# Performance work log

Hardware: AMD Instinct MI355X
Metric: run time of the kernel (lower is better)

Reference implementation:

```python
import jax, jax.numpy as jnp
import numpy as np

N_NODES = 8192
EMBED = 64
N_NEURONS = [512, 256, 128]
ACTION_SIZE = 8
BATCH = 4096


def setup_inputs() -> dict:
    key = jax.random.key(0)
    ks = jax.random.split(key, 16)
    in_size = 2 * N_NODES + 2 * EMBED

    def u(k, shape, bound):
        return jax.random.uniform(k, shape, jnp.float32, -bound, bound)

    stdv1 = 1.0 / np.sqrt(N_NEURONS[0])
    stdv2 = 1.0 / np.sqrt(EMBED)
    return {
        "state": jax.random.uniform(ks[0], (N_NODES, N_NODES), jnp.float32),
        "start": jax.random.randint(ks[1], (BATCH,), 0, N_NODES),
        "end": jax.random.randint(ks[2], (BATCH,), 0, N_NODES),
        # GCN layer params
        "gw1": u(ks[3], (1, N_NEURONS[0]), stdv1),
        "gb1": u(ks[4], (N_NEURONS[0],), stdv1),
        "gw2": u(ks[5], (N_NEURONS[0], EMBED), stdv2),
        "gb2": u(ks[6], (EMBED,), stdv2),
        # dense head params (xavier-ish)
        "fw1": u(ks[7], (in_size, N_NEURONS[0]), np.sqrt(6.0 / (in_size + N_NEURONS[0]))),
        "fb1": jnp.zeros((N_NEURONS[0],), jnp.float32),
        "fw2": u(ks[8], (N_NEURONS[0], N_NEURONS[1]), np.sqrt(6.0 / (N_NEURONS[0] + N_NEURONS[1]))),
        "fb2": jnp.zeros((N_NEURONS[1],), jnp.float32),
        "fw3": u(ks[9], (N_NEURONS[1], N_NEURONS[2]), np.sqrt(6.0 / (N_NEURONS[1] + N_NEURONS[2]))),
        "fb3": jnp.zeros((N_NEURONS[2],), jnp.float32),
        "fw4": u(ks[10], (N_NEURONS[2], ACTION_SIZE), np.sqrt(6.0 / (N_NEURONS[2] + ACTION_SIZE))),
        "fb4": jnp.zeros((ACTION_SIZE,), jnp.float32),
    }


def reference(state, start, end, gw1, gb1, gw2, gb2,
              fw1, fb1, fw2, fb2, fw3, fb3, fw4, fb4):
    # x = diag(state) as [N, 1] node features
    x = jnp.diagonal(state)[:, None]
    # adj = state with zeroed diagonal, detached (no grad through adj)
    adj = jax.lax.stop_gradient(jnp.fill_diagonal(state, 0.0, inplace=False))
    # GCN layer 1: relu(adj @ (x @ W) + b); dropout is identity in eval mode
    h = jax.nn.relu(adj @ (x @ gw1) + gb1)              # [N, 512]
    # GCN layer 2
    h = jax.nn.relu(adj @ (h @ gw2) + gb2)              # [N, 64]
    h = jax.nn.log_softmax(h, axis=1)                   # [N, 64]
    # gather node features and embeddings for each (start, end) edge
    edge_features = jnp.concatenate(
        [state[start], state[end], h[start], h[end]], axis=1)  # [B, 2N+2E]
    y = jax.nn.relu(edge_features @ fw1 + fb1)
    y = jax.nn.relu(y @ fw2 + fb2)                      # d1 dropout: identity (eval)
    y = jax.nn.relu(y @ fw3 + fb3)
    action_q = jax.nn.relu(y @ fw4 + fb4)               # [B, action_size]
    return action_q
```

## Files before the change

kernel.cpp:

```cpp
#include <hip/hip_runtime.h>
#include <hip/hip_bf16.h>
#include <math.h>

#define NN 8192
#define EMB 64
#define H1D 512
#define NB 4096

typedef __bf16 bf16x8 __attribute__((ext_vector_type(8)));
typedef float f32x4 __attribute__((ext_vector_type(4)));
typedef unsigned short u16x8 __attribute__((ext_vector_type(8)));
typedef unsigned short u16x4 __attribute__((ext_vector_type(4)));

__device__ __forceinline__ unsigned short f2bf(float f) {
    return __bfloat16_as_ushort(__float2bfloat16(f));
}

__device__ __forceinline__ void gload16(const void* g, void* l) {
    __builtin_amdgcn_global_load_lds(
        (const __attribute__((address_space(1))) void*)g,
        (__attribute__((address_space(3))) void*)l, 16, 0, 0);
}

__global__ void k_diag(const float* __restrict__ state, float* __restrict__ diag) {
    int i = blockIdx.x * blockDim.x + threadIdx.x;
    if (i < NN) diag[i] = state[(size_t)i * NN + i];
}

__global__ __launch_bounds__(256) void k_convert(const float* __restrict__ state,
                                                 const float* __restrict__ diag,
                                                 unsigned short* __restrict__ stateb,
                                                 float* __restrict__ s) {
    int row = blockIdx.x;
    int tid = threadIdx.x;
    const float4* st4 = (const float4*)(state + (size_t)row * NN);
    const float4* dg4 = (const float4*)diag;
    unsigned short* drow = stateb + (size_t)row * NN;
    float acc = 0.f;
#pragma unroll
    for (int t = 0; t < 8; ++t) {
        int f = t * 256 + tid;
        float4 a = st4[f], d = dg4[f];
        acc += a.x * d.x + a.y * d.y + a.z * d.z + a.w * d.w;
        u16x4 o;
        o[0] = f2bf(a.x); o[1] = f2bf(a.y); o[2] = f2bf(a.z); o[3] = f2bf(a.w);
        *(u16x4*)&drow[f * 4] = o;
    }
#pragma unroll
    for (int m = 32; m >= 1; m >>= 1) acc += __shfl_xor(acc, m);
    __shared__ float red[4];
    if ((tid & 63) == 0) red[tid >> 6] = acc;
    __syncthreads();
    if (tid == 0) {
        float tot = red[0] + red[1] + red[2] + red[3];
        float d = diag[row];
        s[row] = tot - d * d;
    }
}

__global__ __launch_bounds__(256) void k_tr_fw1(const float* __restrict__ fw1,
                                                unsigned short* __restrict__ fw1t) {
    __shared__ float t[64][65];
    int kb = blockIdx.x * 64, nb = blockIdx.y * 64;
    int tid = threadIdx.x;
#pragma unroll
    for (int i = 0; i < 4; ++i) {
        int lin = i * 256 + tid;
        int r = lin >> 4, c4 = (lin & 15) << 2;
        float4 v = *(const float4*)&fw1[(size_t)(kb + r) * 512 + nb + c4];
        t[r][c4] = v.x; t[r][c4 + 1] = v.y; t[r][c4 + 2] = v.z; t[r][c4 + 3] = v.w;
    }
    __syncthreads();
#pragma unroll
    for (int i = 0; i < 4; ++i) {
        int lin = i * 256 + tid;
        int n = lin >> 4, k4 = (lin & 15) << 2;
        u16x4 o;
        o[0] = f2bf(t[k4 + 0][n]); o[1] = f2bf(t[k4 + 1][n]);
        o[2] = f2bf(t[k4 + 2][n]); o[3] = f2bf(t[k4 + 3][n]);
        *(u16x4*)&fw1t[(size_t)(nb + n) * 16512 + kb + k4] = o;
    }
}

__global__ __launch_bounds__(256) void k_tr_q(const float* __restrict__ q,
                                              unsigned short* __restrict__ qbT) {
    __shared__ float t[64][65];
    int kb = blockIdx.x * 64;
    int tid = threadIdx.x;
#pragma unroll
    for (int i = 0; i < 4; ++i) {
        int lin = i * 256 + tid;
        int r = lin >> 4, c4 = (lin & 15) << 2;
        float4 v = *(const float4*)&q[(size_t)(kb + r) * 64 + c4];
        t[r][c4] = v.x; t[r][c4 + 1] = v.y; t[r][c4 + 2] = v.z; t[r][c4 + 3] = v.w;
    }
    __syncthreads();
#pragma unroll
    for (int i = 0; i < 4; ++i) {
        int lin = i * 256 + tid;
        int c = lin >> 4, k4 = (lin & 15) << 2;
        u16x4 o;
        o[0] = f2bf(t[k4 + 0][c]); o[1] = f2bf(t[k4 + 1][c]);
        o[2] = f2bf(t[k4 + 2][c]); o[3] = f2bf(t[k4 + 3][c]);
        *(u16x4*)&qbT[(size_t)c * 8192 + kb + k4] = o;
    }
}

__global__ __launch_bounds__(256) void k_rowdot(const float* __restrict__ state,
                                                const float* __restrict__ diag,
                                                float* __restrict__ s) {
    int row = blockIdx.x;
    int tid = threadIdx.x;
    const float4* st4 = (const float4*)(state + (size_t)row * NN);
    const float4* dg4 = (const float4*)diag;
    float acc = 0.f;
#pragma unroll
    for (int t = 0; t < 8; ++t) {
        int f = t * 256 + tid;
        float4 a = st4[f], d = dg4[f];
        acc += a.x * d.x + a.y * d.y + a.z * d.z + a.w * d.w;
    }
#pragma unroll
    for (int m = 32; m >= 1; m >>= 1) acc += __shfl_xor(acc, m);
    __shared__ float red[4];
    if ((tid & 63) == 0) red[tid >> 6] = acc;
    __syncthreads();
    if (tid == 0) {
        float tot = red[0] + red[1] + red[2] + red[3];
        float d = diag[row];
        s[row] = tot - d * d;
    }
}

__global__ __launch_bounds__(256) void k_q(const float* __restrict__ s,
                                           const float* __restrict__ gw1,
                                           const float* __restrict__ gb1,
                                           const float* __restrict__ gw2,
                                           float* __restrict__ q) {
    int tid = threadIdx.x;
    int c = tid & 63;
    int row = blockIdx.x * 4 + (tid >> 6);
    float sv = s[row];
    float a0 = 0.f, a1 = 0.f, a2 = 0.f, a3 = 0.f;
    for (int j = 0; j < H1D; j += 4) {
        float h0 = fmaxf(fmaf(sv, gw1[j + 0], gb1[j + 0]), 0.f);
        float h1 = fmaxf(fmaf(sv, gw1[j + 1], gb1[j + 1]), 0.f);
        float h2 = fmaxf(fmaf(sv, gw1[j + 2], gb1[j + 2]), 0.f);
        float h3 = fmaxf(fmaf(sv, gw1[j + 3], gb1[j + 3]), 0.f);
        a0 = fmaf(h0, gw2[(j + 0) * EMB + c], a0);
        a1 = fmaf(h1, gw2[(j + 1) * EMB + c], a1);
        a2 = fmaf(h2, gw2[(j + 2) * EMB + c], a2);
        a3 = fmaf(h3, gw2[(j + 3) * EMB + c], a3);
    }
    q[row * EMB + c] = (a0 + a1) + (a2 + a3);
}


__global__ __launch_bounds__(256) void k_gcn2_mfma_b(const unsigned short* __restrict__ stateb,
                                                     const unsigned short* __restrict__ qbT,
                                                     float* __restrict__ partg) {
    __shared__ __align__(16) unsigned short Asm[2][64 * 64];
    __shared__ __align__(16) unsigned short Bsm[2][64 * 64];
    const int tid = threadIdx.x;
    const int l = tid & 63, wv = tid >> 6;
    const int rbase = blockIdx.x * 64;
    const int kbase0 = blockIdx.y * 1024;

    const unsigned short* aP[2]; const unsigned short* bP[2]; int lb[2];
#pragma unroll
    for (int i = 0; i < 2; ++i) {
        int slot = i * 256 + tid;
        int r = slot >> 3, cg = slot & 7;
        aP[i] = stateb + (size_t)(rbase + r) * NN + kbase0 + ((cg ^ (r & 7)) << 3);
        bP[i] = qbT + (size_t)r * 8192 + kbase0 + ((cg ^ (r & 7)) << 3);
        lb[i] = (i * 256 + wv * 64) * 8;
    }

    f32x4 acc[4] = {};
    const int fr = l & 15, fq = l >> 4;

#pragma unroll
    for (int i = 0; i < 2; ++i) {
        gload16(aP[i], &Asm[0][lb[i]]);
        gload16(bP[i], &Bsm[0][lb[i]]);
    }
    __syncthreads();

    int buf = 0;
    for (int kt = 0; kt < 16; ++kt) {
        if (kt < 15) {
#pragma unroll
            for (int i = 0; i < 2; ++i) {
                gload16(aP[i] + (kt + 1) * 64, &Asm[buf ^ 1][lb[i]]);
                gload16(bP[i] + (kt + 1) * 64, &Bsm[buf ^ 1][lb[i]]);
            }
        }
#pragma unroll
        for (int kh = 0; kh < 2; ++kh) {
            int ch = kh * 4 + fq;
            int row = wv * 16 + fr;
            bf16x8 aF = *(const bf16x8*)&Asm[buf][row * 64 + ((ch ^ (row & 7)) << 3)];
            bf16x8 bF[4];
#pragma unroll
            for (int n = 0; n < 4; ++n) {
                int col = n * 16 + fr;
                bF[n] = *(const bf16x8*)&Bsm[buf][col * 64 + ((ch ^ (col & 7)) << 3)];
            }
#pragma unroll
            for (int n = 0; n < 4; ++n)
                acc[n] = __builtin_amdgcn_mfma_f32_16x16x32_bf16(aF, bF[n], acc[n], 0, 0, 0);
        }
        __syncthreads();
        buf ^= 1;
    }

    float* dst = partg + (size_t)blockIdx.y * (NN * EMB);
#pragma unroll
    for (int n = 0; n < 4; ++n) {
        int row0 = rbase + wv * 16 + fq * 4;
        int col = n * 16 + fr;
#pragma unroll
        for (int j = 0; j < 4; ++j)
            dst[(size_t)(row0 + j) * EMB + col] = acc[n][j];
    }
}

__global__ __launch_bounds__(256) void k_gcn2_combine_b(const float* __restrict__ partg,
                                                        const float* __restrict__ diag,
                                                        const float* __restrict__ q,
                                                        const float* __restrict__ gb2,
                                                        unsigned short* __restrict__ hb) {
    int tid = threadIdx.x;
    int c = tid & 63;
    int row = blockIdx.x * 4 + (tid >> 6);
    int idx = row * EMB + c;
    float v = gb2[c] - diag[row] * q[idx];
#pragma unroll
    for (int p = 0; p < 8; ++p) v += partg[(size_t)p * NN * EMB + idx];
    v = fmaxf(v, 0.f);
    float mx = v;
#pragma unroll
    for (int m = 32; m >= 1; m >>= 1) mx = fmaxf(mx, __shfl_xor(mx, m));
    float e = expf(v - mx);
    float sum = e;
#pragma unroll
    for (int m = 32; m >= 1; m >>= 1) sum += __shfl_xor(sum, m);
    hb[idx] = f2bf(v - mx - logf(sum));
}

__global__ __launch_bounds__(256) void k_head1_mfma_b(
    const unsigned short* __restrict__ stateb, const unsigned short* __restrict__ hb,
    const int* __restrict__ start, const int* __restrict__ end,
    const unsigned short* __restrict__ fw1t, float* __restrict__ parth) {
    __shared__ __align__(16) unsigned short Asm[128 * 64];
    __shared__ __align__(16) unsigned short Bsm[128 * 64];
    __shared__ int ridx[128];
    const int tid = threadIdx.x;
    const int l = tid & 63, wv = tid >> 6;
    const int rbase = blockIdx.x * 128, cbase = blockIdx.y * 128;
    const int ks = blockIdx.z, side = ks >> 1, half = ks & 1;
    if (tid < 128) ridx[tid] = (side ? end : start)[rbase + tid];
    __syncthreads();

    const unsigned short* aS[4]; const unsigned short* aH[4];
    const unsigned short* bP[4];
    unsigned short* aL[4]; unsigned short* bL[4];
#pragma unroll
    for (int i = 0; i < 4; ++i) {
        int slot = i * 256 + tid;
        int r = slot >> 3, cg = slot & 7;
        int swz = (cg ^ (r & 7)) << 3;
        int gi = ridx[r];
        aS[i] = stateb + (size_t)gi * NN + half * 4096 + swz;
        aH[i] = hb + gi * EMB + swz;
        bP[i] = fw1t + (size_t)(cbase + r) * 16512 + swz;
        aL[i] = &Asm[slot * 8];
        bL[i] = &Bsm[slot * 8];
    }
    const int kB0 = side * 8192 + half * 4096;
    const int kBtail = 16384 + side * 64;
    const int nsteps = 64 + half;

    f32x4 acc[4][4] = {};
    const int wm = wv >> 1, wn = wv & 1;
    const int fr = l & 15, fq = l >> 4;

    for (int kt = 0; kt < nsteps; ++kt) {
        if (kt < 64) {
#pragma unroll
            for (int i = 0; i < 4; ++i) {
                gload16(aS[i] + kt * 64, aL[i]);
                gload16(bP[i] + kB0 + kt * 64, bL[i]);
            }
        } else {
#pragma unroll
            for (int i = 0; i < 4; ++i) {
                gload16(aH[i], aL[i]);
                gload16(bP[i] + kBtail, bL[i]);
            }
        }
        __syncthreads();
#pragma unroll
        for (int kh = 0; kh < 2; ++kh) {
            int ch = kh * 4 + fq;
            bf16x8 aF[4], bF[4];
#pragma unroll
            for (int m = 0; m < 4; ++m) {
                int row = wm * 64 + m * 16 + fr;
                aF[m] = *(const bf16x8*)&Asm[row * 64 + ((ch ^ (row & 7)) << 3)];
            }
#pragma unroll
            for (int n = 0; n < 4; ++n) {
                int nl = wn * 64 + n * 16 + fr;
                bF[n] = *(const bf16x8*)&Bsm[nl * 64 + ((ch ^ (nl & 7)) << 3)];
            }
#pragma unroll
            for (int m = 0; m < 4; ++m)
#pragma unroll
                for (int n = 0; n < 4; ++n)
                    acc[m][n] = __builtin_amdgcn_mfma_f32_16x16x32_bf16(
                        aF[m], bF[n], acc[m][n], 0, 0, 0);
        }
        __syncthreads();
    }

    float* dst = parth + (size_t)ks * (NB * H1D);
#pragma unroll
    for (int m = 0; m < 4; ++m) {
        int row0 = rbase + wm * 64 + m * 16 + fq * 4;
#pragma unroll
        for (int n = 0; n < 4; ++n) {
            int col = cbase + wn * 64 + n * 16 + fr;
#pragma unroll
            for (int j = 0; j < 4; ++j)
                dst[(size_t)(row0 + j) * H1D + col] = acc[m][n][j];
        }
    }
}

__global__ void k_head1_fin4(const float* __restrict__ parth, const float* __restrict__ fb1,
                             float* __restrict__ y1) {
    int i = blockIdx.x * blockDim.x + threadIdx.x;
    const size_t S = (size_t)NB * H1D;
    float4 a = *(const float4*)&parth[(size_t)i * 4];
    float4 b = *(const float4*)&parth[S + (size_t)i * 4];
    float4 c = *(const float4*)&parth[2 * S + (size_t)i * 4];
    float4 d = *(const float4*)&parth[3 * S + (size_t)i * 4];
    float4 bias = *(const float4*)&fb1[(i * 4) & 511];
    float4 o;
    o.x = fmaxf(a.x + b.x + c.x + d.x + bias.x, 0.f);
    o.y = fmaxf(a.y + b.y + c.y + d.y + bias.y, 0.f);
    o.z = fmaxf(a.z + b.z + c.z + d.z + bias.z, 0.f);
    o.w = fmaxf(a.w + b.w + c.w + d.w + bias.w, 0.f);
    *(float4*)&y1[(size_t)i * 4] = o;
}


__global__ __launch_bounds__(256) void k_gcn2_mfma(const float* __restrict__ state,
                                                   const unsigned short* __restrict__ qbT,
                                                   float* __restrict__ partg) {
    __shared__ __align__(16) unsigned short Asm[2][64 * 64];
    __shared__ __align__(16) unsigned short Bsm[2][64 * 64];
    const int tid = threadIdx.x;
    const int l = tid & 63, wv = tid >> 6;
    const int rbase = blockIdx.x * 64;
    const int kbase0 = blockIdx.y * 1024;

    const float* aptr[2]; int awr[2];
#pragma unroll
    for (int i = 0; i < 2; ++i) {
        int slot = i * 256 + tid;
        int r = slot >> 3, cg = slot & 7;
        aptr[i] = state + (size_t)(rbase + r) * NN + kbase0 + cg * 8;
        awr[i] = r * 64 + ((cg ^ (r & 7)) << 3);
    }
    const unsigned short* bptr[2]; int bbase[2];
#pragma unroll
    for (int i = 0; i < 2; ++i) {
        int c = i * 32 + wv * 8 + (l >> 3);
        int cg = l & 7;
        bptr[i] = qbT + (size_t)c * 8192 + kbase0 + ((cg ^ (c & 7)) << 3);
        bbase[i] = i * 2048 + wv * 512;
    }

    f32x4 acc[4] = {};
    const int fr = l & 15, fq = l >> 4;
    float4 va[2][2];

#pragma unroll
    for (int i = 0; i < 2; ++i) {
        va[i][0] = *(const float4*)aptr[i];
        va[i][1] = *(const float4*)(aptr[i] + 4);
    }
#pragma unroll
    for (int i = 0; i < 2; ++i) {
        u16x8 o;
        o[0] = f2bf(va[i][0].x); o[1] = f2bf(va[i][0].y); o[2] = f2bf(va[i][0].z); o[3] = f2bf(va[i][0].w);
        o[4] = f2bf(va[i][1].x); o[5] = f2bf(va[i][1].y); o[6] = f2bf(va[i][1].z); o[7] = f2bf(va[i][1].w);
        *(u16x8*)&Asm[0][awr[i]] = o;
        gload16(bptr[i], &Bsm[0][bbase[i]]);
    }
    __syncthreads();

    int buf = 0;
    for (int kt = 0; kt < 16; ++kt) {
        if (kt < 15) {
#pragma unroll
            for (int i = 0; i < 2; ++i) {
                gload16(bptr[i] + (kt + 1) * 64, &Bsm[buf ^ 1][bbase[i]]);
                va[i][0] = *(const float4*)(aptr[i] + (kt + 1) * 64);
                va[i][1] = *(const float4*)(aptr[i] + (kt + 1) * 64 + 4);
            }
        }
#pragma unroll
        for (int kh = 0; kh < 2; ++kh) {
            int ch = kh * 4 + fq;
            int row = wv * 16 + fr;
            bf16x8 aF = *(const bf16x8*)&Asm[buf][row * 64 + ((ch ^ (row & 7)) << 3)];
            bf16x8 bF[4];
#pragma unroll
            for (int n = 0; n < 4; ++n) {
                int col = n * 16 + fr;
                bF[n] = *(const bf16x8*)&Bsm[buf][col * 64 + ((ch ^ (col & 7)) << 3)];
            }
#pragma unroll
            for (int n = 0; n < 4; ++n)
                acc[n] = __builtin_amdgcn_mfma_f32_16x16x32_bf16(aF, bF[n], acc[n], 0, 0, 0);
        }
        if (kt < 15) {
#pragma unroll
            for (int i = 0; i < 2; ++i) {
                u16x8 o;
                o[0] = f2bf(va[i][0].x); o[1] = f2bf(va[i][0].y); o[2] = f2bf(va[i][0].z); o[3] = f2bf(va[i][0].w);
                o[4] = f2bf(va[i][1].x); o[5] = f2bf(va[i][1].y); o[6] = f2bf(va[i][1].z); o[7] = f2bf(va[i][1].w);
                *(u16x8*)&Asm[buf ^ 1][awr[i]] = o;
            }
        }
        __syncthreads();
        buf ^= 1;
    }

    float* dst = partg + (size_t)blockIdx.y * (NN * EMB);
#pragma unroll
    for (int n = 0; n < 4; ++n) {
        int row0 = rbase + wv * 16 + fq * 4;
        int col = n * 16 + fr;
#pragma unroll
        for (int j = 0; j < 4; ++j)
            dst[(size_t)(row0 + j) * EMB + col] = acc[n][j];
    }
}

__global__ __launch_bounds__(256) void k_gcn2_combine(const float* __restrict__ partg,
                                                      const float* __restrict__ diag,
                                                      const float* __restrict__ q,
                                                      const float* __restrict__ gb2,
                                                      float* __restrict__ h) {
    int tid = threadIdx.x;
    int c = tid & 63;
    int row = blockIdx.x * 4 + (tid >> 6);
    int idx = row * EMB + c;
    float v = gb2[c] - diag[row] * q[idx];
#pragma unroll
    for (int p = 0; p < 8; ++p) v += partg[(size_t)p * NN * EMB + idx];
    v = fmaxf(v, 0.f);
    float mx = v;
#pragma unroll
    for (int m = 32; m >= 1; m >>= 1) mx = fmaxf(mx, __shfl_xor(mx, m));
    float e = expf(v - mx);
    float sum = e;
#pragma unroll
    for (int m = 32; m >= 1; m >>= 1) sum += __shfl_xor(sum, m);
    h[idx] = v - mx - logf(sum);
}

__global__ __launch_bounds__(256) void k_head1_mfma(
    const float* __restrict__ state, const float* __restrict__ h,
    const int* __restrict__ start, const int* __restrict__ end,
    const unsigned short* __restrict__ fw1t, float* __restrict__ part) {
    __shared__ __align__(16) unsigned short Asm[2][64 * 64];
    __shared__ __align__(16) unsigned short Bsm[2][128 * 64];
    __shared__ int ridx[64];
    const int tid = threadIdx.x;
    const int l = tid & 63, wv = tid >> 6;
    const int rbase = blockIdx.x * 64, cbase = blockIdx.y * 128;
    const int ks = blockIdx.z;
    if (tid < 64) ridx[tid] = (ks ? end : start)[rbase + tid];
    __syncthreads();

    const float* aptr[2]; const float* hptr[2]; int awr[2];
#pragma unroll
    for (int i = 0; i < 2; ++i) {
        int slot = i * 256 + tid;
        int r = slot >> 3, cg = slot & 7;
        int gi = ridx[r];
        aptr[i] = state + (size_t)gi * NN + cg * 8;
        hptr[i] = h + gi * EMB + cg * 8;
        awr[i] = r * 64 + ((cg ^ (r & 7)) << 3);
    }
    const unsigned short* bptr[4]; int bbase[4];
#pragma unroll
    for (int i = 0; i < 4; ++i) {
        int n = i * 32 + wv * 8 + (l >> 3);
        int cg = l & 7;
        bptr[i] = fw1t + (size_t)(cbase + n) * 16512 + ((cg ^ (n & 7)) << 3);
        bbase[i] = i * 2048 + wv * 512;
    }

    f32x4 acc[2][4] = {};
    const int wm = wv >> 1, wn = wv & 1;
    const int fr = l & 15, fq = l >> 4;
    float4 va[2][2];

#pragma unroll
    for (int i = 0; i < 2; ++i) {
        va[i][0] = *(const float4*)aptr[i];
        va[i][1] = *(const float4*)(aptr[i] + 4);
    }
#pragma unroll
    for (int i = 0; i < 2; ++i) {
        u16x8 o;
        o[0] = f2bf(va[i][0].x); o[1] = f2bf(va[i][0].y); o[2] = f2bf(va[i][0].z); o[3] = f2bf(va[i][0].w);
        o[4] = f2bf(va[i][1].x); o[5] = f2bf(va[i][1].y); o[6] = f2bf(va[i][1].z); o[7] = f2bf(va[i][1].w);
        *(u16x8*)&Asm[0][awr[i]] = o;
    }
#pragma unroll
    for (int i = 0; i < 4; ++i) gload16(bptr[i] + ks * 8192, &Bsm[0][bbase[i]]);
    __syncthreads();

    int buf = 0;
    for (int kt = 0; kt < 129; ++kt) {
        if (kt < 128) {
            int nxt = kt + 1;
            int kB = (nxt < 128) ? (ks * 8192 + nxt * 64) : (16384 + ks * 64);
#pragma unroll
            for (int i = 0; i < 4; ++i) gload16(bptr[i] + kB, &Bsm[buf ^ 1][bbase[i]]);
#pragma unroll
            for (int i = 0; i < 2; ++i) {
                const float* src = (nxt < 128) ? (aptr[i] + nxt * 64) : hptr[i];
                va[i][0] = *(const float4*)src;
                va[i][1] = *(const float4*)(src + 4);
            }
        }
#pragma unroll
        for (int kh = 0; kh < 2; ++kh) {
            int ch = kh * 4 + fq;
            bf16x8 aF[2], bF[4];
#pragma unroll
            for (int m = 0; m < 2; ++m) {
                int row = wm * 32 + m * 16 + fr;
                aF[m] = *(const bf16x8*)&Asm[buf][row * 64 + ((ch ^ (row & 7)) << 3)];
            }
#pragma unroll
            for (int n = 0; n < 4; ++n) {
                int nl = wn * 64 + n * 16 + fr;
                bF[n] = *(const bf16x8*)&Bsm[buf][nl * 64 + ((ch ^ (nl & 7)) << 3)];
            }
#pragma unroll
            for (int m = 0; m < 2; ++m)
#pragma unroll
                for (int n = 0; n < 4; ++n)
                    acc[m][n] = __builtin_amdgcn_mfma_f32_16x16x32_bf16(
                        aF[m], bF[n], acc[m][n], 0, 0, 0);
        }
        if (kt < 128) {
#pragma unroll
            for (int i = 0; i < 2; ++i) {
                u16x8 o;
                o[0] = f2bf(va[i][0].x); o[1] = f2bf(va[i][0].y); o[2] = f2bf(va[i][0].z); o[3] = f2bf(va[i][0].w);
                o[4] = f2bf(va[i][1].x); o[5] = f2bf(va[i][1].y); o[6] = f2bf(va[i][1].z); o[7] = f2bf(va[i][1].w);
                *(u16x8*)&Asm[buf ^ 1][awr[i]] = o;
            }
        }
        __syncthreads();
        buf ^= 1;
    }

    float* dst = part + (size_t)ks * (NB * H1D);
#pragma unroll
    for (int m = 0; m < 2; ++m) {
        int row0 = rbase + wm * 32 + m * 16 + fq * 4;
#pragma unroll
        for (int n = 0; n < 4; ++n) {
            int col = cbase + wn * 64 + n * 16 + fr;
#pragma unroll
            for (int j = 0; j < 4; ++j)
                dst[(size_t)(row0 + j) * H1D + col] = acc[m][n][j];
        }
    }
}

__global__ void k_head1_fin(const float* __restrict__ part, const float* __restrict__ fb1,
                            float* __restrict__ y1) {
    int i = blockIdx.x * blockDim.x + threadIdx.x;
    float4 a = *(const float4*)&part[(size_t)i * 4];
    float4 b = *(const float4*)&part[(size_t)NB * H1D + (size_t)i * 4];
    float4 bias = *(const float4*)&fb1[(i * 4) & 511];
    float4 o;
    o.x = fmaxf(a.x + b.x + bias.x, 0.f);
    o.y = fmaxf(a.y + b.y + bias.y, 0.f);
    o.z = fmaxf(a.z + b.z + bias.z, 0.f);
    o.w = fmaxf(a.w + b.w + bias.w, 0.f);
    *(float4*)&y1[(size_t)i * 4] = o;
}

#define GEMM_INNER(AsM, BsM)                                          \
    _Pragma("unroll")                                                 \
    for (int k4 = 0; k4 < 64; k4 += 4) {                              \
        float av[4][4], bv[4][4];                                     \
        _Pragma("unroll")                                             \
        for (int i = 0; i < 4; ++i)                                   \
            *(float4*)av[i] = *(const float4*)&AsM[4 * row_t + i][k4];\
        _Pragma("unroll")                                             \
        for (int t = 0; t < 4; ++t)                                   \
            *(float4*)bv[t] = *(const float4*)&BsM[k4 + t][4 * col_t];\
        _Pragma("unroll")                                             \
        for (int i = 0; i < 4; ++i) {                                 \
            _Pragma("unroll")                                         \
            for (int t = 0; t < 4; ++t) {                             \
                _Pragma("unroll")                                     \
                for (int j = 0; j < 4; ++j)                           \
                    acc[i][j] = fmaf(av[i][t], bv[t][j], acc[i][j]);  \
            }                                                         \
        }                                                             \
    }

__global__ __launch_bounds__(256) void k_gemm_relu(const float* __restrict__ A,
                                                   const float* __restrict__ W,
                                                   const float* __restrict__ bias,
                                                   float* __restrict__ C,
                                                   int M, int N, int K) {
    __shared__ __align__(16) float As[64][68];
    __shared__ __align__(16) float Bs[64][68];
    int tid = threadIdx.x;
    int rbase = blockIdx.x * 64;
    int cbase = blockIdx.y * 64;
    int row_t = tid >> 4, col_t = tid & 15;
    float acc[4][4] = {};
    for (int kt = 0; kt < K / 64; ++kt) {
        int kbase = kt * 64;
#pragma unroll
        for (int l = 0; l < 4; ++l) {
            int lin = l * 256 + tid;
            int r = lin >> 4, k4 = (lin & 15) << 2;
            float4 v = *(const float4*)&A[(size_t)(rbase + r) * K + kbase + k4];
            As[r][k4 + 0] = v.x; As[r][k4 + 1] = v.y; As[r][k4 + 2] = v.z; As[r][k4 + 3] = v.w;
            float4 w = *(const float4*)&W[(size_t)(kbase + r) * N + cbase + k4];
            Bs[r][k4 + 0] = w.x; Bs[r][k4 + 1] = w.y; Bs[r][k4 + 2] = w.z; Bs[r][k4 + 3] = w.w;
        }
        __syncthreads();
        GEMM_INNER(As, Bs)
        __syncthreads();
    }
#pragma unroll
    for (int i = 0; i < 4; ++i) {
        int row = rbase + 4 * row_t + i;
        int col = cbase + 4 * col_t;
        float4 v;
        v.x = fmaxf(acc[i][0] + bias[col + 0], 0.f);
        v.y = fmaxf(acc[i][1] + bias[col + 1], 0.f);
        v.z = fmaxf(acc[i][2] + bias[col + 2], 0.f);
        v.w = fmaxf(acc[i][3] + bias[col + 3], 0.f);
        *(float4*)&C[(size_t)row * N + col] = v;
    }
}

__global__ void k_head4(const float* __restrict__ y3, const float* __restrict__ fw4,
                        const float* __restrict__ fb4, float* __restrict__ out) {
    int tid = blockIdx.x * blockDim.x + threadIdx.x;
    int b = tid >> 3, j = tid & 7;
    float acc = fb4[j];
    for (int k = 0; k < 128; ++k)
        acc = fmaf(y3[b * 128 + k], fw4[k * 8 + j], acc);
    out[tid] = fmaxf(acc, 0.f);
}

extern "C" void kernel_launch(void* const* d_in, const int* in_sizes, int n_in,
                              void* d_out, int out_size, void* d_ws, size_t ws_size,
                              hipStream_t stream) {
    const float* state = (const float*)d_in[0];
    const int* start   = (const int*)d_in[1];
    const int* end     = (const int*)d_in[2];
    const float* gw1   = (const float*)d_in[3];
    const float* gb1   = (const float*)d_in[4];
    const float* gw2   = (const float*)d_in[5];
    const float* gb2   = (const float*)d_in[6];
    const float* fw1   = (const float*)d_in[7];
    const float* fb1   = (const float*)d_in[8];
    const float* fw2   = (const float*)d_in[9];
    const float* fb2   = (const float*)d_in[10];
    const float* fw3   = (const float*)d_in[11];
    const float* fb3   = (const float*)d_in[12];
    const float* fw4   = (const float*)d_in[13];
    const float* fb4   = (const float*)d_in[14];
    float* out = (float*)d_out;
    float* ws = (float*)d_ws;

    const size_t NEED_BIG = 51429376ull * 4ull;
    const size_t NEED_FB  = 9748480ull * 4ull;

    if (ws_size >= NEED_BIG) {
        float* diag = ws;
        float* s    = ws + 8192;
        float* q    = ws + 16384;
        unsigned short* qbT = (unsigned short*)(ws + 540672);
        unsigned short* hb  = (unsigned short*)(ws + 802816);
        float* partg = ws + 1064960;
        unsigned short* fw1t = (unsigned short*)(ws + 5259264);
        unsigned short* stateb = (unsigned short*)(ws + 9486336);
        float* parth = ws + 43040768;
        float* y1   = ws + 5259264;
        float* y2   = ws + 16384;
        float* y3   = ws + 7356416;

        k_diag<<<32, 256, 0, stream>>>(state, diag);
        k_convert<<<8192, 256, 0, stream>>>(state, diag, stateb, s);
        k_tr_fw1<<<dim3(258, 8), 256, 0, stream>>>(fw1, fw1t);
        k_q<<<2048, 256, 0, stream>>>(s, gw1, gb1, gw2, q);
        k_tr_q<<<128, 256, 0, stream>>>(q, qbT);
        k_gcn2_mfma_b<<<dim3(128, 8), 256, 0, stream>>>(stateb, qbT, partg);
        k_gcn2_combine_b<<<2048, 256, 0, stream>>>(partg, diag, q, gb2, hb);
        k_head1_mfma_b<<<dim3(32, 4, 4), 256, 0, stream>>>(stateb, hb, start, end, fw1t, parth);
        k_head1_fin4<<<2048, 256, 0, stream>>>(parth, fb1, y1);
        k_gemm_relu<<<dim3(64, 4), 256, 0, stream>>>(y1, fw2, fb2, y2, NB, 256, 512);
        k_gemm_relu<<<dim3(64, 2), 256, 0, stream>>>(y2, fw3, fb3, y3, NB, 128, 256);
        k_head4<<<128, 256, 0, stream>>>(y3, fw4, fb4, out);
        return;
    }

    if (ws_size < NEED_FB) return;

    float* diag = ws;
    float* s    = ws + 8192;
    float* q    = ws + 16384;
    unsigned short* qbT = (unsigned short*)(ws + 540672);
    float* h    = ws + 802816;
    float* partg = ws + 1327104;
    unsigned short* fw1t = (unsigned short*)(ws + 5521408);
    float* parth = ws + 1327104;
    float* y1   = ws + 5521408;
    float* y2   = ws + 16384;
    float* y3   = ws + 7618560;

    k_diag<<<32, 256, 0, stream>>>(state, diag);
    k_tr_fw1<<<dim3(258, 8), 256, 0, stream>>>(fw1, fw1t);
    k_rowdot<<<8192, 256, 0, stream>>>(state, diag, s);
    k_q<<<2048, 256, 0, stream>>>(s, gw1, gb1, gw2, q);
    k_tr_q<<<128, 256, 0, stream>>>(q, qbT);
    k_gcn2_mfma<<<dim3(128, 8), 256, 0, stream>>>(state, qbT, partg);
    k_gcn2_combine<<<2048, 256, 0, stream>>>(partg, diag, q, gb2, h);
    k_head1_mfma<<<dim3(64, 4, 2), 256, 0, stream>>>(state, h, start, end, fw1t, parth);
    k_head1_fin<<<2048, 256, 0, stream>>>(parth, fb1, y1);
    k_gemm_relu<<<dim3(64, 4), 256, 0, stream>>>(y1, fw2, fb2, y2, NB, 256, 512);
    k_gemm_relu<<<dim3(64, 2), 256, 0, stream>>>(y2, fw3, fb3, y3, NB, 128, 256);
    k_head4<<<128, 256, 0, stream>>>(y3, fw4, fb4, out);
}
```

Measured before the change: 293.9 us.

## Enlarge GCN2 row tile and split head1 K into eight partial slices

```diff
diff --git a/kernel.cpp b/kernel.cpp
--- a/kernel.cpp
+++ b/kernel.cpp
@@ -159,56 +159,67 @@
 __global__ __launch_bounds__(256) void k_gcn2_mfma_b(const unsigned short* __restrict__ stateb,
                                                      const unsigned short* __restrict__ qbT,
                                                      float* __restrict__ partg) {
-    __shared__ __align__(16) unsigned short Asm[2][64 * 64];
+    __shared__ __align__(16) unsigned short Asm[2][128 * 64];
     __shared__ __align__(16) unsigned short Bsm[2][64 * 64];
     const int tid = threadIdx.x;
     const int l = tid & 63, wv = tid >> 6;
-    const int rbase = blockIdx.x * 64;
+    const int rbase = blockIdx.x * 128;
     const int kbase0 = blockIdx.y * 1024;
 
-    const unsigned short* aP[2]; const unsigned short* bP[2]; int lb[2];
-#pragma unroll
-    for (int i = 0; i < 2; ++i) {
+    const unsigned short* aP[4]; int aLo[4];
+#pragma unroll
+    for (int i = 0; i < 4; ++i) {
         int slot = i * 256 + tid;
         int r = slot >> 3, cg = slot & 7;
         aP[i] = stateb + (size_t)(rbase + r) * NN + kbase0 + ((cg ^ (r & 7)) << 3);
-        bP[i] = qbT + (size_t)r * 8192 + kbase0 + ((cg ^ (r & 7)) << 3);
-        lb[i] = (i * 256 + wv * 64) * 8;
-    }
-
-    f32x4 acc[4] = {};
+        aLo[i] = slot * 8;
+    }
+    const unsigned short* bP[2]; int bLo[2];
+#pragma unroll
+    for (int i = 0; i < 2; ++i) {
+        int slot = i * 256 + tid;
+        int c = slot >> 3, cg = slot & 7;
+        bP[i] = qbT + (size_t)c * 8192 + kbase0 + ((cg ^ (c & 7)) << 3);
+        bLo[i] = slot * 8;
+    }
+
+    f32x4 acc[2][4] = {};
     const int fr = l & 15, fq = l >> 4;
 
 #pragma unroll
-    for (int i = 0; i < 2; ++i) {
-        gload16(aP[i], &Asm[0][lb[i]]);
-        gload16(bP[i], &Bsm[0][lb[i]]);
-    }
+    for (int i = 0; i < 4; ++i) gload16(aP[i], &Asm[0][aLo[i]]);
+#pragma unroll
+    for (int i = 0; i < 2; ++i) gload16(bP[i], &Bsm[0][bLo[i]]);
     __syncthreads();
 
     int buf = 0;
     for (int kt = 0; kt < 16; ++kt) {
         if (kt < 15) {
 #pragma unroll
-            for (int i = 0; i < 2; ++i) {
-                gload16(aP[i] + (kt + 1) * 64, &Asm[buf ^ 1][lb[i]]);
-                gload16(bP[i] + (kt + 1) * 64, &Bsm[buf ^ 1][lb[i]]);
-            }
+            for (int i = 0; i < 4; ++i) gload16(aP[i] + (kt + 1) * 64, &Asm[buf ^ 1][aLo[i]]);
+#pragma unroll
+            for (int i = 0; i < 2; ++i) gload16(bP[i] + (kt + 1) * 64, &Bsm[buf ^ 1][bLo[i]]);
         }
 #pragma unroll
         for (int kh = 0; kh < 2; ++kh) {
             int ch = kh * 4 + fq;
-            int row = wv * 16 + fr;
-            bf16x8 aF = *(const bf16x8*)&Asm[buf][row * 64 + ((ch ^ (row & 7)) << 3)];
-            bf16x8 bF[4];
+            bf16x8 aF[2], bF[4];
+#pragma unroll
+            for (int m = 0; m < 2; ++m) {
+                int row = wv * 32 + m * 16 + fr;
+                aF[m] = *(const bf16x8*)&Asm[buf][row * 64 + ((ch ^ (row & 7)) << 3)];
+            }
 #pragma unroll
             for (int n = 0; n < 4; ++n) {
                 int col = n * 16 + fr;
                 bF[n] = *(const bf16x8*)&Bsm[buf][col * 64 + ((ch ^ (col & 7)) << 3)];
             }
 #pragma unroll
-            for (int n = 0; n < 4; ++n)
-                acc[n] = __builtin_amdgcn_mfma_f32_16x16x32_bf16(aF, bF[n], acc[n], 0, 0, 0);
+            for (int m = 0; m < 2; ++m)
+#pragma unroll
+                for (int n = 0; n < 4; ++n)
+                    acc[m][n] = __builtin_amdgcn_mfma_f32_16x16x32_bf16(
+                        aF[m], bF[n], acc[m][n], 0, 0, 0);
         }
         __syncthreads();
         buf ^= 1;
@@ -216,12 +227,15 @@
 
     float* dst = partg + (size_t)blockIdx.y * (NN * EMB);
 #pragma unroll
-    for (int n = 0; n < 4; ++n) {
-        int row0 = rbase + wv * 16 + fq * 4;
-        int col = n * 16 + fr;
-#pragma unroll
-        for (int j = 0; j < 4; ++j)
-            dst[(size_t)(row0 + j) * EMB + col] = acc[n][j];
+    for (int m = 0; m < 2; ++m) {
+        int row0 = rbase + wv * 32 + m * 16 + fq * 4;
+#pragma unroll
+        for (int n = 0; n < 4; ++n) {
+            int col = n * 16 + fr;
+#pragma unroll
+            for (int j = 0; j < 4; ++j)
+                dst[(size_t)(row0 + j) * EMB + col] = acc[m][n][j];
+        }
     }
 }
 
@@ -258,7 +272,7 @@
     const int tid = threadIdx.x;
     const int l = tid & 63, wv = tid >> 6;
     const int rbase = blockIdx.x * 128, cbase = blockIdx.y * 128;
-    const int ks = blockIdx.z, side = ks >> 1, half = ks & 1;
+    const int ks = blockIdx.z, side = ks >> 2, quarter = ks & 3;
     if (tid < 128) ridx[tid] = (side ? end : start)[rbase + tid];
     __syncthreads();
 
@@ -271,22 +285,22 @@
         int r = slot >> 3, cg = slot & 7;
         int swz = (cg ^ (r & 7)) << 3;
         int gi = ridx[r];
-        aS[i] = stateb + (size_t)gi * NN + half * 4096 + swz;
+        aS[i] = stateb + (size_t)gi * NN + quarter * 2048 + swz;
         aH[i] = hb + gi * EMB + swz;
         bP[i] = fw1t + (size_t)(cbase + r) * 16512 + swz;
         aL[i] = &Asm[slot * 8];
         bL[i] = &Bsm[slot * 8];
     }
-    const int kB0 = side * 8192 + half * 4096;
+    const int kB0 = side * 8192 + quarter * 2048;
     const int kBtail = 16384 + side * 64;
-    const int nsteps = 64 + half;
+    const int nsteps = 32 + (quarter == 3 ? 1 : 0);
 
     f32x4 acc[4][4] = {};
     const int wm = wv >> 1, wn = wv & 1;
     const int fr = l & 15, fq = l >> 4;
 
     for (int kt = 0; kt < nsteps; ++kt) {
-        if (kt < 64) {
+        if (kt < 32) {
 #pragma unroll
             for (int i = 0; i < 4; ++i) {
                 gload16(aS[i] + kt * 64, aL[i]);
@@ -338,20 +352,22 @@
     }
 }
 
-__global__ void k_head1_fin4(const float* __restrict__ parth, const float* __restrict__ fb1,
+__global__ void k_head1_fin8(const float* __restrict__ parth, const float* __restrict__ fb1,
                              float* __restrict__ y1) {
     int i = blockIdx.x * blockDim.x + threadIdx.x;
     const size_t S = (size_t)NB * H1D;
-    float4 a = *(const float4*)&parth[(size_t)i * 4];
-    float4 b = *(const float4*)&parth[S + (size_t)i * 4];
-    float4 c = *(const float4*)&parth[2 * S + (size_t)i * 4];
-    float4 d = *(const float4*)&parth[3 * S + (size_t)i * 4];
+    float4 acc = *(const float4*)&parth[(size_t)i * 4];
+#pragma unroll
+    for (int p = 1; p < 8; ++p) {
+        float4 v = *(const float4*)&parth[p * S + (size_t)i * 4];
+        acc.x += v.x; acc.y += v.y; acc.z += v.z; acc.w += v.w;
+    }
     float4 bias = *(const float4*)&fb1[(i * 4) & 511];
     float4 o;
-    o.x = fmaxf(a.x + b.x + c.x + d.x + bias.x, 0.f);
-    o.y = fmaxf(a.y + b.y + c.y + d.y + bias.y, 0.f);
-    o.z = fmaxf(a.z + b.z + c.z + d.z + bias.z, 0.f);
-    o.w = fmaxf(a.w + b.w + c.w + d.w + bias.w, 0.f);
+    o.x = fmaxf(acc.x + bias.x, 0.f);
+    o.y = fmaxf(acc.y + bias.y, 0.f);
+    o.z = fmaxf(acc.z + bias.z, 0.f);
+    o.w = fmaxf(acc.w + bias.w, 0.f);
     *(float4*)&y1[(size_t)i * 4] = o;
 }
 
@@ -696,7 +712,7 @@
     float* out = (float*)d_out;
     float* ws = (float*)d_ws;
 
-    const size_t NEED_BIG = 51429376ull * 4ull;
+    const size_t NEED_BIG = 59817984ull * 4ull;
     const size_t NEED_FB  = 9748480ull * 4ull;
 
     if (ws_size >= NEED_BIG) {
@@ -718,10 +734,10 @@
         k_tr_fw1<<<dim3(258, 8), 256, 0, stream>>>(fw1, fw1t);
         k_q<<<2048, 256, 0, stream>>>(s, gw1, gb1, gw2, q);
         k_tr_q<<<128, 256, 0, stream>>>(q, qbT);
-        k_gcn2_mfma_b<<<dim3(128, 8), 256, 0, stream>>>(stateb, qbT, partg);
+        k_gcn2_mfma_b<<<dim3(64, 8), 256, 0, stream>>>(stateb, qbT, partg);
         k_gcn2_combine_b<<<2048, 256, 0, stream>>>(partg, diag, q, gb2, hb);
-        k_head1_mfma_b<<<dim3(32, 4, 4), 256, 0, stream>>>(stateb, hb, start, end, fw1t, parth);
-        k_head1_fin4<<<2048, 256, 0, stream>>>(parth, fb1, y1);
+        k_head1_mfma_b<<<dim3(32, 4, 8), 256, 0, stream>>>(stateb, hb, start, end, fw1t, parth);
+        k_head1_fin8<<<2048, 256, 0, stream>>>(parth, fb1, y1);
         k_gemm_relu<<<dim3(64, 4), 256, 0, stream>>>(y1, fw2, fb2, y2, NB, 256, 512);
         k_gemm_relu<<<dim3(64, 2), 256, 0, stream>>>(y2, fw3, fb3, y3, NB, 128, 256);
         k_head4<<<128, 256, 0, stream>>>(y3, fw4, fb4, out);
```

After: 302.3 us. 2.8% more time.

## Run dense head layers 2 and 3 as bf16 MFMA GEMMs

Applied to the files above, without the earlier changes.

```diff
diff --git a/kernel.cpp b/kernel.cpp
--- a/kernel.cpp
+++ b/kernel.cpp
@@ -79,6 +79,31 @@
         o[0] = f2bf(t[k4 + 0][n]); o[1] = f2bf(t[k4 + 1][n]);
         o[2] = f2bf(t[k4 + 2][n]); o[3] = f2bf(t[k4 + 3][n]);
         *(u16x4*)&fw1t[(size_t)(nb + n) * 16512 + kb + k4] = o;
+    }
+}
+
+__global__ __launch_bounds__(256) void k_tr_w(const float* __restrict__ W,
+                                              unsigned short* __restrict__ Wt,
+                                              int K, int N) {
+    __shared__ float t[64][65];
+    int kb = blockIdx.x * 64, nb = blockIdx.y * 64;
+    int tid = threadIdx.x;
+#pragma unroll
+    for (int i = 0; i < 4; ++i) {
+        int lin = i * 256 + tid;
+        int r = lin >> 4, c4 = (lin & 15) << 2;
+        float4 v = *(const float4*)&W[(size_t)(kb + r) * N + nb + c4];
+        t[r][c4] = v.x; t[r][c4 + 1] = v.y; t[r][c4 + 2] = v.z; t[r][c4 + 3] = v.w;
+    }
+    __syncthreads();
+#pragma unroll
+    for (int i = 0; i < 4; ++i) {
+        int lin = i * 256 + tid;
+        int n = lin >> 4, k4 = (lin & 15) << 2;
+        u16x4 o;
+        o[0] = f2bf(t[k4 + 0][n]); o[1] = f2bf(t[k4 + 1][n]);
+        o[2] = f2bf(t[k4 + 2][n]); o[3] = f2bf(t[k4 + 3][n]);
+        *(u16x4*)&Wt[(size_t)(nb + n) * K + kb + k4] = o;
     }
 }
 
@@ -173,7 +198,7 @@
         int r = slot >> 3, cg = slot & 7;
         aP[i] = stateb + (size_t)(rbase + r) * NN + kbase0 + ((cg ^ (r & 7)) << 3);
         bP[i] = qbT + (size_t)r * 8192 + kbase0 + ((cg ^ (r & 7)) << 3);
-        lb[i] = (i * 256 + wv * 64) * 8;
+        lb[i] = slot * 8;
     }
 
     f32x4 acc[4] = {};
@@ -339,7 +364,7 @@
 }
 
 __global__ void k_head1_fin4(const float* __restrict__ parth, const float* __restrict__ fb1,
-                             float* __restrict__ y1) {
+                             unsigned short* __restrict__ y1b) {
     int i = blockIdx.x * blockDim.x + threadIdx.x;
     const size_t S = (size_t)NB * H1D;
     float4 a = *(const float4*)&parth[(size_t)i * 4];
@@ -347,12 +372,156 @@
     float4 c = *(const float4*)&parth[2 * S + (size_t)i * 4];
     float4 d = *(const float4*)&parth[3 * S + (size_t)i * 4];
     float4 bias = *(const float4*)&fb1[(i * 4) & 511];
-    float4 o;
-    o.x = fmaxf(a.x + b.x + c.x + d.x + bias.x, 0.f);
-    o.y = fmaxf(a.y + b.y + c.y + d.y + bias.y, 0.f);
-    o.z = fmaxf(a.z + b.z + c.z + d.z + bias.z, 0.f);
-    o.w = fmaxf(a.w + b.w + c.w + d.w + bias.w, 0.f);
-    *(float4*)&y1[(size_t)i * 4] = o;
+    u16x4 o;
+    o[0] = f2bf(fmaxf(a.x + b.x + c.x + d.x + bias.x, 0.f));
+    o[1] = f2bf(fmaxf(a.y + b.y + c.y + d.y + bias.y, 0.f));
+    o[2] = f2bf(fmaxf(a.z + b.z + c.z + d.z + bias.z, 0.f));
+    o[3] = f2bf(fmaxf(a.w + b.w + c.w + d.w + bias.w, 0.f));
+    *(u16x4*)&y1b[(size_t)i * 4] = o;
+}
+
+__global__ __launch_bounds__(256) void k_ff1(const unsigned short* __restrict__ A,
+                                             const unsigned short* __restrict__ Wt,
+                                             const float* __restrict__ bias,
+                                             unsigned short* __restrict__ out) {
+    __shared__ __align__(16) unsigned short Asm[128 * 64];
+    __shared__ __align__(16) unsigned short Bsm[128 * 64];
+    const int tid = threadIdx.x;
+    const int l = tid & 63, wv = tid >> 6;
+    const int rbase = blockIdx.x * 128, cbase = blockIdx.y * 128;
+
+    const unsigned short* aP[4]; const unsigned short* bP[4];
+    unsigned short* aL[4]; unsigned short* bL[4];
+#pragma unroll
+    for (int i = 0; i < 4; ++i) {
+        int slot = i * 256 + tid;
+        int r = slot >> 3, cg = slot & 7;
+        int swz = (cg ^ (r & 7)) << 3;
+        aP[i] = A + (size_t)(rbase + r) * 512 + swz;
+        bP[i] = Wt + (size_t)(cbase + r) * 512 + swz;
+        aL[i] = &Asm[slot * 8];
+        bL[i] = &Bsm[slot * 8];
+    }
+
+    f32x4 acc[4][4] = {};
+    const int wm = wv >> 1, wn = wv & 1;
+    const int fr = l & 15, fq = l >> 4;
+
+    for (int kt = 0; kt < 8; ++kt) {
+#pragma unroll
+        for (int i = 0; i < 4; ++i) {
+            gload16(aP[i] + kt * 64, aL[i]);
+            gload16(bP[i] + kt * 64, bL[i]);
+        }
+        __syncthreads();
+#pragma unroll
+        for (int kh = 0; kh < 2; ++kh) {
+            int ch = kh * 4 + fq;
+            bf16x8 aF[4], bF[4];
+#pragma unroll
+            for (int m = 0; m < 4; ++m) {
+                int row = wm * 64 + m * 16 + fr;
+                aF[m] = *(const bf16x8*)&Asm[row * 64 + ((ch ^ (row & 7)) << 3)];
+            }
+#pragma unroll
+            for (int n = 0; n < 4; ++n) {
+                int nl = wn * 64 + n * 16 + fr;
+                bF[n] = *(const bf16x8*)&Bsm[nl * 64 + ((ch ^ (nl & 7)) << 3)];
+            }
+#pragma unroll
+            for (int m = 0; m < 4; ++m)
+#pragma unroll
+                for (int n = 0; n < 4; ++n)
+                    acc[m][n] = __builtin_amdgcn_mfma_f32_16x16x32_bf16(
+                        aF[m], bF[n], acc[m][n], 0, 0, 0);
+        }
+        __syncthreads();
+    }
+
+#pragma unroll
+    for (int m = 0; m < 4; ++m) {
+        int row0 = rbase + wm * 64 + m * 16 + fq * 4;
+#pragma unroll
+        for (int n = 0; n < 4; ++n) {
+            int col = cbase + wn * 64 + n * 16 + fr;
+            float bv = bias[col];
+#pragma unroll
+            for (int j = 0; j < 4; ++j)
+                out[(size_t)(row0 + j) * 256 + col] = f2bf(fmaxf(acc[m][n][j] + bv, 0.f));
+        }
+    }
+}
+
+__global__ __launch_bounds__(256) void k_ff2(const unsigned short* __restrict__ A,
+                                             const unsigned short* __restrict__ Wt,
+                                             const float* __restrict__ bias,
+                                             float* __restrict__ out) {
+    __shared__ __align__(16) unsigned short Asm[128 * 64];
+    __shared__ __align__(16) unsigned short Bsm[128 * 64];
+    const int tid = threadIdx.x;
+    const int l = tid & 63, wv = tid >> 6;
+    const int rbase = blockIdx.x * 128, cbase = 0;
+
+    const unsigned short* aP[4]; const unsigned short* bP[4];
+    unsigned short* aL[4]; unsigned short* bL[4];
+#pragma unroll
+    for (int i = 0; i < 4; ++i) {
+        int slot = i * 256 + tid;
+        int r = slot >> 3, cg = slot & 7;
+        int swz = (cg ^ (r & 7)) << 3;
+        aP[i] = A + (size_t)(rbase + r) * 256 + swz;
+        bP[i] = Wt + (size_t)(cbase + r) * 256 + swz;
+        aL[i] = &Asm[slot * 8];
+        bL[i] = &Bsm[slot * 8];
+    }
+
+    f32x4 acc[4][4] = {};
+    const int wm = wv >> 1, wn = wv & 1;
+    const int fr = l & 15, fq = l >> 4;
+
+    for (int kt = 0; kt < 4; ++kt) {
+#pragma unroll
+        for (int i = 0; i < 4; ++i) {
+            gload16(aP[i] + kt * 64, aL[i]);
+            gload16(bP[i] + kt * 64, bL[i]);
+        }
+        __syncthreads();
+#pragma unroll
+        for (int kh = 0; kh < 2; ++kh) {
+            int ch = kh * 4 + fq;
+            bf16x8 aF[4], bF[4];
+#pragma unroll
+            for (int m = 0; m < 4; ++m) {
+                int row = wm * 64 + m * 16 + fr;
+                aF[m] = *(const bf16x8*)&Asm[row * 64 + ((ch ^ (row & 7)) << 3)];
+            }
+#pragma unroll
+            for (int n = 0; n < 4; ++n) {
+                int nl = wn * 64 + n * 16 + fr;
+                bF[n] = *(const bf16x8*)&Bsm[nl * 64 + ((ch ^ (nl & 7)) << 3)];
+            }
+#pragma unroll
+            for (int m = 0; m < 4; ++m)
+#pragma unroll
+                for (int n = 0; n < 4; ++n)
+                    acc[m][n] = __builtin_amdgcn_mfma_f32_16x16x32_bf16(
+                        aF[m], bF[n], acc[m][n], 0, 0, 0);
+        }
+        __syncthreads();
+    }
+
+#pragma unroll
+    for (int m = 0; m < 4; ++m) {
+        int row0 = rbase + wm * 64 + m * 16 + fq * 4;
+#pragma unroll
+        for (int n = 0; n < 4; ++n) {
+            int col = cbase + wn * 64 + n * 16 + fr;
+            float bv = bias[col];
+#pragma unroll
+            for (int j = 0; j < 4; ++j)
+                out[(size_t)(row0 + j) * 128 + col] = fmaxf(acc[m][n][j] + bv, 0.f);
+        }
+    }
 }
 
 
@@ -696,7 +865,7 @@
     float* out = (float*)d_out;
     float* ws = (float*)d_ws;
 
-    const size_t NEED_BIG = 51429376ull * 4ull;
+    const size_t NEED_BIG = 53084160ull * 4ull;
     const size_t NEED_FB  = 9748480ull * 4ull;
 
     if (ws_size >= NEED_BIG) {
@@ -709,21 +878,25 @@
         unsigned short* fw1t = (unsigned short*)(ws + 5259264);
         unsigned short* stateb = (unsigned short*)(ws + 9486336);
         float* parth = ws + 43040768;
-        float* y1   = ws + 5259264;
-        float* y2   = ws + 16384;
+        unsigned short* fw2t = (unsigned short*)(ws + 51429376);
+        unsigned short* fw3t = (unsigned short*)(ws + 51494912);
+        unsigned short* y1b  = (unsigned short*)(ws + 51511296);
+        unsigned short* y2b  = (unsigned short*)(ws + 52559872);
         float* y3   = ws + 7356416;
 
         k_diag<<<32, 256, 0, stream>>>(state, diag);
         k_convert<<<8192, 256, 0, stream>>>(state, diag, stateb, s);
         k_tr_fw1<<<dim3(258, 8), 256, 0, stream>>>(fw1, fw1t);
+        k_tr_w<<<dim3(8, 4), 256, 0, stream>>>(fw2, fw2t, 512, 256);
+        k_tr_w<<<dim3(4, 2), 256, 0, stream>>>(fw3, fw3t, 256, 128);
         k_q<<<2048, 256, 0, stream>>>(s, gw1, gb1, gw2, q);
         k_tr_q<<<128, 256, 0, stream>>>(q, qbT);
         k_gcn2_mfma_b<<<dim3(128, 8), 256, 0, stream>>>(stateb, qbT, partg);
         k_gcn2_combine_b<<<2048, 256, 0, stream>>>(partg, diag, q, gb2, hb);
         k_head1_mfma_b<<<dim3(32, 4, 4), 256, 0, stream>>>(stateb, hb, start, end, fw1t, parth);
-        k_head1_fin4<<<2048, 256, 0, stream>>>(parth, fb1, y1);
-        k_gemm_relu<<<dim3(64, 4), 256, 0, stream>>>(y1, fw2, fb2, y2, NB, 256, 512);
-        k_gemm_relu<<<dim3(64, 2), 256, 0, stream>>>(y2, fw3, fb3, y3, NB, 128, 256);
+        k_head1_fin4<<<2048, 256, 0, stream>>>(parth, fb1, y1b);
+        k_ff1<<<dim3(32, 2), 256, 0, stream>>>(y1b, fw2t, fb2, y2b);
+        k_ff2<<<dim3(32, 1), 256, 0, stream>>>(y2b, fw3t, fb3, y3);
         k_head4<<<128, 256, 0, stream>>>(y3, fw4, fb4, out);
         return;
     }
```

Measured after the change: 279.7 us. 4.8% less time.
